# Optimization experiments

Measured on AMD Instinct MI355X. Metric: run time of the kernel, lower is better.

Reference implementation:

```python
import jax, jax.numpy as jnp
import numpy as np

B, K, W = 16, 64, 2048
D, DH, DFF, NL, V = 512, 256, 2048, 4, 32001
LN_EPS = 1e-5


def _ln(x, g, b):
    mu = jnp.mean(x, axis=-1, keepdims=True)
    var = jnp.mean(jnp.square(x - mu), axis=-1, keepdims=True)
    return (x - mu) * jax.lax.rsqrt(var + LN_EPS) * g + b


def setup_inputs() -> dict:
    key = jax.random.key(0)
    ks = iter(jax.random.split(key, 64))
    nrm = lambda shape, s=0.02: (jax.random.normal(next(ks), shape, dtype=jnp.float32) * s)
    inp = {
        "cache": jax.random.randint(next(ks), (B, K), 0, V),
        "seq": jax.random.randint(next(ks), (B, W), 0, V),
        "item_embed": nrm((V, D)),
        "cache_pos_embed": nrm((K, D)),
        "seq_pos_embed": nrm((W, D)),
        "segment_embed": nrm((2, D)),
        # per-layer stacked params (leading dim NL)
        "wq_s": nrm((NL, D, DH)), "wk_s": nrm((NL, D, DH)), "wv_s": nrm((NL, D, DH)),
        "wq_c": nrm((NL, D, DH)), "wk_c": nrm((NL, D, DH)), "wv_c": nrm((NL, D, DH)),
        "w_out": nrm((NL, D, D)), "b_out": jnp.zeros((NL, D), jnp.float32),
        "ln1_g": jnp.ones((NL, D), jnp.float32), "ln1_b": jnp.zeros((NL, D), jnp.float32),
        "ln2_g": jnp.ones((NL, D), jnp.float32), "ln2_b": jnp.zeros((NL, D), jnp.float32),
        "w_ff1": nrm((NL, D, DFF)), "b_ff1": jnp.zeros((NL, DFF), jnp.float32),
        "w_ff2": nrm((NL, DFF, D)), "b_ff2": jnp.zeros((NL, D), jnp.float32),
        "fin_g": jnp.ones((D,), jnp.float32), "fin_b": jnp.zeros((D,), jnp.float32),
        "w_ev": nrm((D, 1)), "b_ev": jnp.zeros((1,), jnp.float32),
    }
    return inp


def _forward(cache, seq, item_embed, cache_pos_embed, seq_pos_embed, segment_embed,
             wq_s, wk_s, wv_s, wq_c, wk_c, wv_c, w_out, b_out,
             ln1_g, ln1_b, ln2_g, ln2_b, w_ff1, b_ff1, w_ff2, b_ff2,
             fin_g, fin_b, w_ev, b_ev):
    scale = 1.0 / jnp.sqrt(jnp.float32(DH))
    cache_emb = item_embed[cache] + cache_pos_embed[None, :, :] + segment_embed[0]
    seq_emb = item_embed[seq] + seq_pos_embed[None, :, :] + segment_embed[1]
    h = jnp.concatenate([cache_emb, seq_emb], axis=1)  # (B, K+W, D)
    L = K + W
    # additive mask for stream a: cache rows attend to all seq tokens,
    # seq rows are causal within the window.  (L, W)
    causal = jnp.triu(jnp.full((W, W), -jnp.inf, dtype=jnp.float32), k=1)
    mask_a = jnp.concatenate([jnp.zeros((K, W), jnp.float32), causal], axis=0)

    for l in range(NL):
        hn = _ln(h, ln1_g[l], ln1_b[l])
        hn_seq = hn[:, K:]
        hn_cache = hn[:, :K]
        # stream a: all tokens query the sequence window (causal for seq rows)
        q_a = hn @ wq_s[l]
        k_a = hn_seq @ wk_s[l]
        v_a = hn_seq @ wv_s[l]
        scores_a = jnp.einsum('bld,bwd->blw', q_a, k_a) * scale + mask_a
        out_a = jnp.einsum('blw,bwd->bld', jax.nn.softmax(scores_a, axis=-1), v_a)
        # stream b: all tokens query the cache slots (full attention)
        q_b = hn @ wq_c[l]
        k_b = hn_cache @ wk_c[l]
        v_b = hn_cache @ wv_c[l]
        scores_b = jnp.einsum('bld,bkd->blk', q_b, k_b) * scale
        out_b = jnp.einsum('blk,bkd->bld', jax.nn.softmax(scores_b, axis=-1), v_b)
        attn_out = jnp.concatenate([out_a, out_b], axis=-1)  # (B, L, D)
        h = h + attn_out @ w_out[l] + b_out[l]
        hn2 = _ln(h, ln2_g[l], ln2_b[l])
        h = h + jax.nn.relu(hn2 @ w_ff1[l] + b_ff1[l]) @ w_ff2[l] + b_ff2[l]

    h = _ln(h, fin_g, fin_b)
    logits = (h[:, :K] @ w_ev + b_ev)[..., 0]  # (B, K)
    return logits


def reference(cache, seq, item_embed, cache_pos_embed, seq_pos_embed, segment_embed,
              wq_s, wk_s, wv_s, wq_c, wk_c, wv_c, w_out, b_out,
              ln1_g, ln1_b, ln2_g, ln2_b, w_ff1, b_ff1, w_ff2, b_ff2,
              fin_g, fin_b, w_ev, b_ev):
    return _forward(cache, seq, item_embed, cache_pos_embed, seq_pos_embed, segment_embed,
                    wq_s, wk_s, wv_s, wq_c, wk_c, wv_c, w_out, b_out,
                    ln1_g, ln1_b, ln2_g, ln2_b, w_ff1, b_ff1, w_ff2, b_ff2,
                    fin_g, fin_b, w_ev, b_ev)
```

## Files before the change

### kernel.cpp

```cpp
#include <hip/hip_runtime.h>
#include <hip/hip_bf16.h>
#include <cstdint>

#define CB 16
#define CK 64
#define CW 2048
#define CL 2112
#define CD 512
#define CDH 256
#define CDFF 2048
#define CNL 4
#define CROWS (CB*CL)
#define NCH 2
#define RCH2 (CROWS/NCH)

typedef __attribute__((ext_vector_type(8))) short bf16x8;
typedef __attribute__((ext_vector_type(4))) float f32x4;

__device__ __forceinline__ float bf2f(unsigned short u) {
    union { unsigned int i; float f; } x; x.i = ((unsigned int)u) << 16; return x.f;
}

__device__ __forceinline__ void load_lds16(const void* g, void* l) {
    __builtin_amdgcn_global_load_lds(
        (const __attribute__((address_space(1))) void*)g,
        (__attribute__((address_space(3))) void*)l, 16, 0, 0);
}

__device__ __forceinline__ void xcd_swizzle(int& bx, int& by) {
    const int gx = gridDim.x, nwg = gx * gridDim.y;
    if ((nwg & 7) == 0) {
        const int flat = by * gx + bx;
        const int cpx = nwg >> 3;
        const int swz = (flat & 7) * cpx + (flat >> 3);
        bx = swz % gx; by = swz / gx;
    }
}

#define BM 128
#define BN 128
#define BKG 64

__global__ __launch_bounds__(256) void gemm_bt(
    const short* __restrict__ A, const short* __restrict__ Bt, void* __restrict__ C,
    const float* __restrict__ bias, int M, int N, int Kd,
    int lda, int ldb, int ldc, long sA, long sB, long sC, float scale, int epi,
    int ksplit)
{
    __shared__ short lA[2][BM * BKG];
    __shared__ short lB[2][BN * BKG];
    const int tid = threadIdx.x;
    const int wave = tid >> 6, lane = tid & 63;
    const int wy = wave >> 1, wx = wave & 1;
    const int lr = lane & 15, quad = lane >> 4;
    int bx = blockIdx.x, by = blockIdx.y;
    xcd_swizzle(bx, by);
    const int m0 = by * BM, n0 = bx * BN;
    const int z = blockIdx.z;
    const short* Ab = A + (size_t)z * sA;
    const short* Bb = Bt + (size_t)z * sB;

    f32x4 acc[4][4];
#pragma unroll
    for (int i = 0; i < 4; i++)
#pragma unroll
        for (int j = 0; j < 4; j++) acc[i][j] = (f32x4){0.f, 0.f, 0.f, 0.f};

    const int sRow = lane >> 3;
    const int sCol = (((lane & 7) ^ sRow) << 3);

    int kbeg = 0, kend = Kd;
    if (ksplit > 1) { const int kc = Kd / ksplit; kbeg = z * kc; kend = kbeg + kc; }
    const int nsteps = (kend - kbeg) / BKG;

    auto stage = [&](int buf, int k0) {
#pragma unroll
        for (int n = 0; n < 4; ++n) {
            const int c = wave * 4 + n;
            int ar = m0 + c * 8 + sRow; if (ar > M - 1) ar = M - 1;
            load_lds16(Ab + (size_t)ar * lda + k0 + sCol, &lA[buf][c * 512]);
            int br = n0 + c * 8 + sRow; if (br > N - 1) br = N - 1;
            load_lds16(Bb + (size_t)br * ldb + k0 + sCol, &lB[buf][c * 512]);
        }
    };

    stage(0, kbeg);
    for (int t = 0; t < nsteps; ++t) {
        const int cur = t & 1;
        if (t + 1 < nsteps) {
            stage(cur ^ 1, kbeg + (t + 1) * BKG);
            asm volatile("s_waitcnt vmcnt(8)\n\ts_barrier" ::: "memory");
        } else {
            asm volatile("s_waitcnt vmcnt(0)\n\ts_barrier" ::: "memory");
        }
#pragma unroll
        for (int kk = 0; kk < BKG; kk += 32) {
            const int k4 = kk >> 3;
            bf16x8 av[4], bv[4];
#pragma unroll
            for (int i = 0; i < 4; i++) {
                const int ri = wy * 64 + i * 16 + lr;
                av[i] = *(const bf16x8*)&lA[cur][ri * BKG + ((((k4 + quad) ^ (ri & 7)) << 3))];
            }
#pragma unroll
            for (int j = 0; j < 4; j++) {
                const int rj = wx * 64 + j * 16 + lr;
                bv[j] = *(const bf16x8*)&lB[cur][rj * BKG + ((((k4 + quad) ^ (rj & 7)) << 3))];
            }
#pragma unroll
            for (int i = 0; i < 4; i++)
#pragma unroll
                for (int j = 0; j < 4; j++)
                    acc[i][j] = __builtin_amdgcn_mfma_f32_16x16x32_bf16(av[i], bv[j], acc[i][j], 0, 0, 0);
        }
        asm volatile("s_barrier" ::: "memory");
    }

    const int colBase = n0 + wx * 64 + lr;
    if (epi == 3) {
        float* Cp = (float*)C + (size_t)z * sC;
#pragma unroll
        for (int i = 0; i < 4; i++) {
            const int row0 = m0 + wy * 64 + i * 16 + quad * 4;
#pragma unroll
            for (int j = 0; j < 4; j++) {
                const int col = colBase + j * 16;
                if (col >= N) continue;
                const float bv_ = bias ? bias[col] : 0.f;
#pragma unroll
                for (int r = 0; r < 4; r++) {
                    const int row = row0 + r;
                    if (row < M) Cp[(size_t)row * ldc + col] += acc[i][j][r] + bv_;
                }
            }
        }
    } else {
        __hip_bfloat16* Cp = (__hip_bfloat16*)C + (size_t)z * sC;
#pragma unroll
        for (int i = 0; i < 4; i++) {
            const int row0 = m0 + wy * 64 + i * 16 + quad * 4;
#pragma unroll
            for (int j = 0; j < 4; j++) {
                const int col = colBase + j * 16;
                if (col >= N) continue;
                const float bv_ = (epi == 1) ? bias[col] : 0.f;
#pragma unroll
                for (int r = 0; r < 4; r++) {
                    const int row = row0 + r;
                    if (row < M) {
                        float v = acc[i][j][r];
                        if (epi == 1) { v += bv_; v = v > 0.f ? v : 0.f; }
                        else if (epi == 2) v *= scale;
                        Cp[(size_t)row * ldc + col] = __float2bfloat16(v);
                    }
                }
            }
        }
    }
}

__global__ __launch_bounds__(256, 2) void flash_a(
    const short* __restrict__ q,
    const short* __restrict__ ka,
    const short* __restrict__ vt,
    short* __restrict__ out)
{
    __shared__ short kbuf[64 * 256];
    __shared__ short vbuf[256 * 64];
    __shared__ short pbuf[64 * 64];
    const int tid = threadIdx.x, wave = tid >> 6, lane = tid & 63;
    const int lr = lane & 15, quad = lane >> 4;

    const int id = blockIdx.x;
    const int x = id & 7, k = id >> 3;
    const int b = 2 * x + (k >= 33);
    const int mi = (k >= 33) ? (k - 33) : k;
    const int mt = (mi == 0) ? 0 : (33 - mi);
    const int m0 = mt * 64;
    const short* kab = ka + (size_t)b * 2048 * 256;
    const short* vtb = vt + (size_t)b * 256 * 2048;

    const int nkt = (mt == 0) ? 32 : mt;

    bf16x8 qf[8];
    {
        const int qr = m0 + wave * 16 + lr;
        const short* p0 = q + ((size_t)b * CL + qr) * 512;
#pragma unroll
        for (int s = 0; s < 8; ++s) qf[s] = *(const bf16x8*)(p0 + s * 32 + quad * 8);
    }

    auto stageK = [&](int kt) {
#pragma unroll
        for (int u = 0; u < 8; ++u) {
            const int seg = u * 4 + wave;
            const int idx = seg * 64 + lane;
            const int row = idx >> 5, cp = idx & 31;
            const int cs = cp ^ (row & 7);
            load_lds16(kab + (size_t)(kt * 64 + row) * 256 + cs * 8, kbuf + seg * 512);
        }
    };
    auto stageV = [&](int kt) {
#pragma unroll
        for (int u = 0; u < 8; ++u) {
            const int seg = u * 4 + wave;
            const int idx = seg * 64 + lane;
            const int row = idx >> 3, cp = idx & 7;
            const int cs = cp ^ (row & 7);
            load_lds16(vtb + (size_t)row * 2048 + kt * 64 + cs * 8, vbuf + seg * 512);
        }
    };

    f32x4 acc_o[16];
#pragma unroll
    for (int jd = 0; jd < 16; jd++) acc_o[jd] = (f32x4){0.f, 0.f, 0.f, 0.f};
    float m_run[4], l_run[4];
    int limit[4];
#pragma unroll
    for (int rr = 0; rr < 4; rr++) {
        m_run[rr] = -1e30f; l_run[rr] = 0.f;
        const int trow = m0 + wave * 16 + quad * 4 + rr;
        limit[rr] = (trow < CK) ? CW : (trow - (CK - 1));
    }

    for (int kt = 0; kt < nkt; ++kt) {
        stageK(kt);
        stageV(kt);
        __syncthreads();

        f32x4 s_[4];
#pragma unroll
        for (int j = 0; j < 4; j++) s_[j] = (f32x4){0.f, 0.f, 0.f, 0.f};
#pragma unroll
        for (int s = 0; s < 8; ++s) {
#pragma unroll
            for (int j = 0; j < 4; ++j) {
                const int rj = j * 16 + lr;
                const bf16x8 bv = *(const bf16x8*)&kbuf[rj * 256 + (((s * 4 + quad) ^ (rj & 7)) << 3)];
                s_[j] = __builtin_amdgcn_mfma_f32_16x16x32_bf16(qf[s], bv, s_[j], 0, 0, 0);
            }
        }

        const int kbase = kt * 64;
        float tmax[4];
#pragma unroll
        for (int rr = 0; rr < 4; rr++) tmax[rr] = -1e30f;
#pragma unroll
        for (int j = 0; j < 4; j++) {
            const int key = kbase + j * 16 + lr;
#pragma unroll
            for (int rr = 0; rr < 4; rr++) {
                const float v = (key < limit[rr]) ? s_[j][rr] * 0.0625f : -1e30f;
                s_[j][rr] = v;
                tmax[rr] = fmaxf(tmax[rr], v);
            }
        }
#pragma unroll
        for (int rr = 0; rr < 4; rr++) {
#pragma unroll
            for (int off = 1; off < 16; off <<= 1)
                tmax[rr] = fmaxf(tmax[rr], __shfl_xor(tmax[rr], off));
        }
        float scal[4], rowsum[4];
#pragma unroll
        for (int rr = 0; rr < 4; rr++) {
            const float mn = fmaxf(m_run[rr], tmax[rr]);
            scal[rr] = __expf(m_run[rr] - mn);
            m_run[rr] = mn;
            rowsum[rr] = 0.f;
        }
#pragma unroll
        for (int j = 0; j < 4; j++) {
            const int cch = j * 2 + (lr >> 3);
#pragma unroll
            for (int rr = 0; rr < 4; rr++) {
                const float e = __expf(s_[j][rr] - m_run[rr]);
                rowsum[rr] += e;
                const float eo = __shfl_xor(e, 1);
                const __hip_bfloat16 b0 = __float2bfloat16(e);
                const __hip_bfloat16 b1 = __float2bfloat16(eo);
                const unsigned pk = ((unsigned)(*(const unsigned short*)&b1) << 16)
                                  | (unsigned)(*(const unsigned short*)&b0);
                if (!(lane & 1)) {
                    const int prow = wave * 16 + quad * 4 + rr;
                    *(unsigned*)&pbuf[prow * 64 + ((cch ^ (prow & 7)) << 3) + (lr & 6)] = pk;
                }
            }
        }
#pragma unroll
        for (int rr = 0; rr < 4; rr++) {
#pragma unroll
            for (int off = 1; off < 16; off <<= 1)
                rowsum[rr] += __shfl_xor(rowsum[rr], off);
            l_run[rr] = l_run[rr] * scal[rr] + rowsum[rr];
        }
#pragma unroll
        for (int jd = 0; jd < 16; jd++)
#pragma unroll
            for (int rr = 0; rr < 4; rr++) acc_o[jd][rr] *= scal[rr];


        const int pr = wave * 16 + lr;
#pragma unroll
        for (int s2 = 0; s2 < 2; ++s2) {
            const bf16x8 pa = *(const bf16x8*)&pbuf[pr * 64 + (((s2 * 4 + quad) ^ (pr & 7)) << 3)];
#pragma unroll
            for (int jd = 0; jd < 16; ++jd) {
                const int rj = jd * 16 + lr;
                const bf16x8 bv = *(const bf16x8*)&vbuf[rj * 64 + (((s2 * 4 + quad) ^ (rj & 7)) << 3)];
                acc_o[jd] = __builtin_amdgcn_mfma_f32_16x16x32_bf16(pa, bv, acc_o[jd], 0, 0, 0);
            }
        }
        __syncthreads();
    }

#pragma unroll
    for (int rr = 0; rr < 4; rr++) {
        const int trow = m0 + wave * 16 + quad * 4 + rr;
        const float rinv = 1.f / l_run[rr];
        __hip_bfloat16* op = (__hip_bfloat16*)out + ((size_t)b * CL + trow) * CD;
#pragma unroll
        for (int jd = 0; jd < 16; jd++)
            op[jd * 16 + lr] = __float2bfloat16(acc_o[jd][rr] * rinv);
    }
}

__global__ void embed_kernel(const int* __restrict__ cache, const int* __restrict__ seq,
                             const float* __restrict__ item, const float* __restrict__ cpos,
                             const float* __restrict__ spos, const float* __restrict__ seg,
                             float* __restrict__ h)
{
    const int row = blockIdx.x;
    const int b = row / CL, t = row - b * CL;
    const int d = threadIdx.x * 4;
    int id; const float* pos; const float* sg;
    if (t < CK) { id = cache[b * CK + t]; pos = cpos + (size_t)t * CD; sg = seg; }
    else { const int tt = t - CK; id = seq[b * CW + tt]; pos = spos + (size_t)tt * CD; sg = seg + CD; }
    const float4 ev = *(const float4*)(item + (size_t)id * CD + d);
    const float4 pv = *(const float4*)(pos + d);
    const float4 sv = *(const float4*)(sg + d);
    float4 r; r.x = ev.x + pv.x + sv.x; r.y = ev.y + pv.y + sv.y;
    r.z = ev.z + pv.z + sv.z; r.w = ev.w + pv.w + sv.w;
    *(float4*)(h + (size_t)row * CD + d) = r;
}

__global__ __launch_bounds__(256) void ln_kernel(const float* __restrict__ h, const float* __restrict__ g,
                                                 const float* __restrict__ bb, __hip_bfloat16* __restrict__ out)
{
    const int row = blockIdx.x * 4 + (threadIdx.x >> 6);
    const int lane = threadIdx.x & 63;
    const float* x = h + (size_t)row * CD + lane * 8;
    const float4 a = *(const float4*)(x);
    const float4 c = *(const float4*)(x + 4);
    float s  = a.x + a.y + a.z + a.w + c.x + c.y + c.z + c.w;
    float s2 = a.x*a.x + a.y*a.y + a.z*a.z + a.w*a.w
             + c.x*c.x + c.y*c.y + c.z*c.z + c.w*c.w;
#pragma unroll
    for (int off = 32; off; off >>= 1) {
        s  += __shfl_xor(s, off);
        s2 += __shfl_xor(s2, off);
    }
    const float mu = s * (1.f / CD);
    const float var = s2 * (1.f / CD) - mu * mu;
    const float rs = rsqrtf(var + 1e-5f);
    const float4 g0 = *(const float4*)(g + lane * 8);
    const float4 g1 = *(const float4*)(g + lane * 8 + 4);
    const float4 b0 = *(const float4*)(bb + lane * 8);
    const float4 b1 = *(const float4*)(bb + lane * 8 + 4);
    float v[8] = { (a.x-mu)*rs*g0.x + b0.x, (a.y-mu)*rs*g0.y + b0.y,
                   (a.z-mu)*rs*g0.z + b0.z, (a.w-mu)*rs*g0.w + b0.w,
                   (c.x-mu)*rs*g1.x + b1.x, (c.y-mu)*rs*g1.y + b1.y,
                   (c.z-mu)*rs*g1.z + b1.z, (c.w-mu)*rs*g1.w + b1.w };
    bf16x8 ov;
#pragma unroll
    for (int kk = 0; kk < 8; kk++) {
        const __hip_bfloat16 hb = __float2bfloat16(v[kk]);
        ov[kk] = *(const short*)&hb;
    }
    *(bf16x8*)(out + (size_t)row * CD + lane * 8) = ov;
}

__global__ __launch_bounds__(256) void softmax_b_kernel(__hip_bfloat16* __restrict__ sb)
{
    const int row = blockIdx.x * 4 + (threadIdx.x >> 6);
    const int lane = threadIdx.x & 63;
    __hip_bfloat16* pr = sb + (size_t)row * 64;
    float x = __bfloat162float(pr[lane]);
    float m = x;
#pragma unroll
    for (int off = 32; off; off >>= 1) m = fmaxf(m, __shfl_xor(m, off));
    const float e = __expf(x - m);
    float s = e;
#pragma unroll
    for (int off = 32; off; off >>= 1) s += __shfl_xor(s, off);
    pr[lane] = __float2bfloat16(e / s);
}

__global__ __launch_bounds__(256) void final_kernel(const float* __restrict__ h, const float* __restrict__ g,
                                                    const float* __restrict__ bb, const float* __restrict__ wev,
                                                    const float* __restrict__ bev, float* __restrict__ out)
{
    const int idx = blockIdx.x;
    const int b = idx >> 6, t = idx & 63;
    const float* x = h + ((size_t)b * CL + t) * CD;
    const int tid = threadIdx.x, wv = tid >> 6, lane = tid & 63;
    const float2 v = *(const float2*)(x + tid * 2);
    float s = v.x + v.y, s2 = v.x * v.x + v.y * v.y;
    __shared__ float red[8];
#pragma unroll
    for (int off = 32; off; off >>= 1) { s += __shfl_down(s, off); s2 += __shfl_down(s2, off); }
    if (lane == 0) { red[wv] = s; red[4 + wv] = s2; }
    __syncthreads();
    s = red[0] + red[1] + red[2] + red[3];
    s2 = red[4] + red[5] + red[6] + red[7];
    const float mu = s * (1.f / CD);
    const float var = s2 * (1.f / CD) - mu * mu;
    const float rs = rsqrtf(var + 1e-5f);
    const float2 gg = *(const float2*)(g + tid * 2);
    const float2 bv = *(const float2*)(bb + tid * 2);
    const float2 wv2 = *(const float2*)(wev + tid * 2);
    float val = ((v.x - mu) * rs * gg.x + bv.x) * wv2.x + ((v.y - mu) * rs * gg.y + bv.y) * wv2.y;
#pragma unroll
    for (int off = 32; off; off >>= 1) val += __shfl_down(val, off);
    __syncthreads();
    if (lane == 0) red[wv] = val;
    __syncthreads();
    if (tid == 0) out[idx] = red[0] + red[1] + red[2] + red[3] + bev[0];
}

__global__ void transpose_f32(const float* __restrict__ in, __hip_bfloat16* __restrict__ out,
                              int R, int Cc, long inzs, long outzs)
{
    __shared__ float tile[32][33];
    const size_t zi = (size_t)blockIdx.z * inzs;
    const size_t zo = (size_t)blockIdx.z * outzs;
    const int c0 = blockIdx.x * 32, r0 = blockIdx.y * 32;
    const int tx = threadIdx.x, ty = threadIdx.y;
#pragma unroll
    for (int i = ty; i < 32; i += 8)
        tile[i][tx] = in[zi + (size_t)(r0 + i) * Cc + c0 + tx];
    __syncthreads();
#pragma unroll
    for (int i = ty; i < 32; i += 8)
        out[zo + (size_t)(c0 + i) * R + r0 + tx] = __float2bfloat16(tile[tx][i]);
}

extern "C" void kernel_launch(void* const* d_in, const int* in_sizes, int n_in,
                              void* d_out, int out_size, void* d_ws, size_t ws_size,
                              hipStream_t stream)
{
    const int*   cache = (const int*)d_in[0];
    const int*   seq   = (const int*)d_in[1];
    const float* item  = (const float*)d_in[2];
    const float* cpos  = (const float*)d_in[3];
    const float* spos  = (const float*)d_in[4];
    const float* seg   = (const float*)d_in[5];
    const float* wq_s  = (const float*)d_in[6];
    const float* wk_s  = (const float*)d_in[7];
    const float* wv_s  = (const float*)d_in[8];
    const float* wq_c  = (const float*)d_in[9];
    const float* wk_c  = (const float*)d_in[10];
    const float* wv_c  = (const float*)d_in[11];
    const float* w_out = (const float*)d_in[12];
    const float* b_out = (const float*)d_in[13];
    const float* ln1_g = (const float*)d_in[14];
    const float* ln1_b = (const float*)d_in[15];
    const float* ln2_g = (const float*)d_in[16];
    const float* ln2_b = (const float*)d_in[17];
    const float* w_ff1 = (const float*)d_in[18];
    const float* b_ff1 = (const float*)d_in[19];
    const float* w_ff2 = (const float*)d_in[20];
    const float* b_ff2 = (const float*)d_in[21];
    const float* fin_g = (const float*)d_in[22];
    const float* fin_b = (const float*)d_in[23];
    const float* w_ev  = (const float*)d_in[24];
    const float* b_ev  = (const float*)d_in[25];

    char* p = (char*)d_ws;
    auto alloc = [&](size_t bytes) { char* r = p; p += (bytes + 255) & ~(size_t)255; return (void*)r; };
    float* h    = (float*)alloc((size_t)CROWS * CD * 4);
    short* hnat = (short*)alloc((size_t)CROWS * CD * 2);
    short* q    = (short*)alloc((size_t)CROWS * 512 * 2);
    short* ka   = (short*)alloc((size_t)CB * CW * CDH * 2);
    short* vt   = (short*)alloc((size_t)CB * CDH * CW * 2);
    short* kb   = (short*)alloc((size_t)CB * 64 * CDH * 2);
    short* vbT  = (short*)alloc((size_t)CB * CDH * 64 * 2);
    short* sb   = (short*)alloc((size_t)CB * CL * 64 * 2);
    short* big  = (short*)alloc((size_t)4 * CL * CW * 2);
    short* wqT  = (short*)alloc((size_t)CNL * 512 * CD * 2);
    short* wksT = (short*)alloc((size_t)CNL * CDH * CD * 2);
    short* wvsT = (short*)alloc((size_t)CNL * CDH * CD * 2);
    short* wkcT = (short*)alloc((size_t)CNL * CDH * CD * 2);
    short* wvcT = (short*)alloc((size_t)CNL * CDH * CD * 2);
    short* woT  = (short*)alloc((size_t)CNL * CD * CD * 2);
    short* wf1T = (short*)alloc((size_t)CNL * CDFF * CD * 2);
    short* wf2T = (short*)alloc((size_t)CNL * CD * CDFF * 2);
    short* ffbig = q;
    (void)big;

    const dim3 tb(32, 8);
    const long zqk = (long)CD * CDH;
    const long zqT = (long)512 * CD;
    transpose_f32<<<dim3(CDH/32, CD/32, CNL), tb, 0, stream>>>(wq_s, (__hip_bfloat16*)wqT, CD, CDH, zqk, zqT);
    transpose_f32<<<dim3(CDH/32, CD/32, CNL), tb, 0, stream>>>(wq_c, (__hip_bfloat16*)(wqT + (size_t)CDH * CD), CD, CDH, zqk, zqT);
    transpose_f32<<<dim3(CDH/32, CD/32, CNL), tb, 0, stream>>>(wk_s, (__hip_bfloat16*)wksT, CD, CDH, zqk, zqk);
    transpose_f32<<<dim3(CDH/32, CD/32, CNL), tb, 0, stream>>>(wv_s, (__hip_bfloat16*)wvsT, CD, CDH, zqk, zqk);
    transpose_f32<<<dim3(CDH/32, CD/32, CNL), tb, 0, stream>>>(wk_c, (__hip_bfloat16*)wkcT, CD, CDH, zqk, zqk);
    transpose_f32<<<dim3(CDH/32, CD/32, CNL), tb, 0, stream>>>(wv_c, (__hip_bfloat16*)wvcT, CD, CDH, zqk, zqk);
    transpose_f32<<<dim3(CD/32, CD/32, CNL), tb, 0, stream>>>(w_out, (__hip_bfloat16*)woT, CD, CD, (long)CD*CD, (long)CD*CD);
    transpose_f32<<<dim3(CDFF/32, CD/32, CNL), tb, 0, stream>>>(w_ff1, (__hip_bfloat16*)wf1T, CD, CDFF, (long)CD*CDFF, (long)CD*CDFF);
    transpose_f32<<<dim3(CD/32, CDFF/32, CNL), tb, 0, stream>>>(w_ff2, (__hip_bfloat16*)wf2T, CDFF, CD, (long)CD*CDFF, (long)CD*CDFF);

    embed_kernel<<<CROWS, 128, 0, stream>>>(cache, seq, item, cpos, spos, seg, h);

    const int mtilesR = CROWS / 128;
    const int mtilesL = (CL + 127) / 128;

    for (int l = 0; l < CNL; ++l) {
        const short* wqTl  = wqT  + (size_t)l * 512 * CD;
        const short* wksTl = wksT + (size_t)l * CDH * CD;
        const short* wvsTl = wvsT + (size_t)l * CDH * CD;
        const short* wkcTl = wkcT + (size_t)l * CDH * CD;
        const short* wvcTl = wvcT + (size_t)l * CDH * CD;
        const short* woTl  = woT  + (size_t)l * CD * CD;
        const short* wf1Tl = wf1T + (size_t)l * CDFF * CD;
        const short* wf2Tl = wf2T + (size_t)l * CD * CDFF;

        ln_kernel<<<CROWS / 4, 256, 0, stream>>>(h, ln1_g + l * CD, ln1_b + l * CD, (__hip_bfloat16*)hnat);

        gemm_bt<<<dim3(512/128, mtilesR, 1), 256, 0, stream>>>(hnat, wqTl, q, nullptr,
            CROWS, 512, CD, CD, CD, 512, 0, 0, 0, 1.f, 0, 1);
        gemm_bt<<<dim3(CDH/128, CW/128, CB), 256, 0, stream>>>(hnat + (size_t)CK * CD, wksTl, ka, nullptr,
            CW, CDH, CD, CD, CD, CDH, (long)CL * CD, 0, (long)CW * CDH, 1.f, 0, 1);
        gemm_bt<<<dim3(CDH/128, 1, CB), 256, 0, stream>>>(hnat, wkcTl, kb, nullptr,
            64, CDH, CD, CD, CD, CDH, (long)CL * CD, 0, (long)64 * CDH, 1.f, 0, 1);
        gemm_bt<<<dim3(1, CDH/128, CB), 256, 0, stream>>>(wvcTl, hnat, vbT, nullptr,
            CDH, 64, CD, CD, CD, 64, 0, (long)CL * CD, (long)CDH * 64, 1.f, 0, 1);
        gemm_bt<<<dim3(CW/128, CDH/128, CB), 256, 0, stream>>>(wvsTl, hnat + (size_t)CK * CD, vt, nullptr,
            CDH, CW, CD, CD, CD, CW, 0, (long)CL * CD, (long)CDH * CW, 1.f, 0, 1);

        gemm_bt<<<dim3(1, mtilesL, CB), 256, 0, stream>>>(q + CDH, kb, sb, nullptr,
            CL, 64, CDH, 512, CDH, 64, (long)CL * 512, (long)64 * CDH, (long)CL * 64, 0.0625f, 2, 1);
        softmax_b_kernel<<<(CB * CL) / 4, 256, 0, stream>>>((__hip_bfloat16*)sb);
        gemm_bt<<<dim3(CDH/128, mtilesL, CB), 256, 0, stream>>>(sb, vbT, hnat + CDH, nullptr,
            CL, CDH, 64, 64, 64, CD, (long)CL * 64, (long)CDH * 64, (long)CL * CD, 1.f, 0, 1);

        flash_a<<<dim3(528), 256, 0, stream>>>(q, ka, vt, hnat);

        gemm_bt<<<dim3(CD/128, mtilesR, 1), 256, 0, stream>>>(hnat, woTl, h, b_out + l * CD,
            CROWS, CD, CD, CD, CD, CD, 0, 0, 0, 1.f, 3, 1);

        ln_kernel<<<CROWS / 4, 256, 0, stream>>>(h, ln2_g + l * CD, ln2_b + l * CD, (__hip_bfloat16*)hnat);

        for (int c = 0; c < NCH; ++c) {
            const size_t r0 = (size_t)c * RCH2;
            gemm_bt<<<dim3(CDFF/128, RCH2/128, 1), 256, 0, stream>>>(hnat + r0 * CD, wf1Tl, ffbig, b_ff1 + l * CDFF,
                RCH2, CDFF, CD, CD, CD, CDFF, 0, 0, 0, 1.f, 1, 1);
            gemm_bt<<<dim3(CD/128, RCH2/128, 1), 256, 0, stream>>>(ffbig, wf2Tl, h + r0 * CD, b_ff2 + l * CD,
                RCH2, CD, CDFF, CDFF, CDFF, CD, 0, 0, 0, 1.f, 3, 1);
        }
    }

    final_kernel<<<CB * CK, 256, 0, stream>>>(h, fin_g, fin_b, w_ev, b_ev, (float*)d_out);
}
```

Before: 3.347 ms.

## Fuse cache-slot attention stream into the flash attention kernel

The second attention stream (queries attending to the 64 cache slots), previously computed as three launches (scores GEMM, softmax kernel, PV GEMM), now runs at the end of the flash_a kernel. Each block stages the per-batch cache K and transposed V into the already allocated LDS buffers, does a single-tile softmax in registers, and writes the second half of the attention output directly. This removes two launches per layer and the round trip of the score matrix through global memory. The cost is extra serial work in the tail of each flash block, on top of its existing load imbalance.

Result: no change. 3.305 ms, median of 2 (-1.3%).

```diff
diff --git a/kernel.cpp b/kernel.cpp
--- a/kernel.cpp
+++ b/kernel.cpp
@@ -163,6 +163,8 @@
     const short* __restrict__ q,
     const short* __restrict__ ka,
     const short* __restrict__ vt,
+    const short* __restrict__ kb,
+    const short* __restrict__ vbT,
     short* __restrict__ out)
 {
     __shared__ short kbuf[64 * 256];
@@ -179,12 +181,14 @@
     const int m0 = mt * 64;
     const short* kab = ka + (size_t)b * 2048 * 256;
     const short* vtb = vt + (size_t)b * 256 * 2048;
+    const short* kbb = kb + (size_t)b * 64 * 256;
+    const short* vbb = vbT + (size_t)b * 256 * 64;
 
     const int nkt = (mt == 0) ? 32 : mt;
 
     bf16x8 qf[8];
+    const int qr = m0 + wave * 16 + lr;
     {
-        const int qr = m0 + wave * 16 + lr;
         const short* p0 = q + ((size_t)b * CL + qr) * 512;
 #pragma unroll
         for (int s = 0; s < 8; ++s) qf[s] = *(const bf16x8*)(p0 + s * 32 + quad * 8);
@@ -208,6 +212,26 @@
             const int row = idx >> 3, cp = idx & 7;
             const int cs = cp ^ (row & 7);
             load_lds16(vtb + (size_t)row * 2048 + kt * 64 + cs * 8, vbuf + seg * 512);
+        }
+    };
+    auto stageKB = [&]() {
+#pragma unroll
+        for (int u = 0; u < 8; ++u) {
+            const int seg = u * 4 + wave;
+            const int idx = seg * 64 + lane;
+            const int row = idx >> 5, cp = idx & 31;
+            const int cs = cp ^ (row & 7);
+            load_lds16(kbb + (size_t)row * 256 + cs * 8, kbuf + seg * 512);
+        }
+    };
+    auto stageVB = [&]() {
+#pragma unroll
+        for (int u = 0; u < 8; ++u) {
+            const int seg = u * 4 + wave;
+            const int idx = seg * 64 + lane;
+            const int row = idx >> 3, cp = idx & 7;
+            const int cs = cp ^ (row & 7);
+            load_lds16(vbb + (size_t)row * 64 + cs * 8, vbuf + seg * 512);
         }
     };
 
@@ -314,6 +338,9 @@
         __syncthreads();
     }
 
+    stageKB();
+    stageVB();
+
 #pragma unroll
     for (int rr = 0; rr < 4; rr++) {
         const int trow = m0 + wave * 16 + quad * 4 + rr;
@@ -322,6 +349,92 @@
 #pragma unroll
         for (int jd = 0; jd < 16; jd++)
             op[jd * 16 + lr] = __float2bfloat16(acc_o[jd][rr] * rinv);
+    }
+
+    {
+        const short* p0 = q + ((size_t)b * CL + qr) * 512 + CDH;
+#pragma unroll
+        for (int s = 0; s < 8; ++s) qf[s] = *(const bf16x8*)(p0 + s * 32 + quad * 8);
+    }
+    __syncthreads();
+
+    {
+        f32x4 s_[4];
+#pragma unroll
+        for (int j = 0; j < 4; j++) s_[j] = (f32x4){0.f, 0.f, 0.f, 0.f};
+#pragma unroll
+        for (int s = 0; s < 8; ++s) {
+#pragma unroll
+            for (int j = 0; j < 4; ++j) {
+                const int rj = j * 16 + lr;
+                const bf16x8 bv = *(const bf16x8*)&kbuf[rj * 256 + (((s * 4 + quad) ^ (rj & 7)) << 3)];
+                s_[j] = __builtin_amdgcn_mfma_f32_16x16x32_bf16(qf[s], bv, s_[j], 0, 0, 0);
+            }
+        }
+        float tmax[4] = {-1e30f, -1e30f, -1e30f, -1e30f};
+#pragma unroll
+        for (int j = 0; j < 4; j++)
+#pragma unroll
+            for (int rr = 0; rr < 4; rr++) {
+                const float v = s_[j][rr] * 0.0625f;
+                s_[j][rr] = v;
+                tmax[rr] = fmaxf(tmax[rr], v);
+            }
+#pragma unroll
+        for (int rr = 0; rr < 4; rr++) {
+#pragma unroll
+            for (int off = 1; off < 16; off <<= 1)
+                tmax[rr] = fmaxf(tmax[rr], __shfl_xor(tmax[rr], off));
+        }
+        float rowsum[4] = {0.f, 0.f, 0.f, 0.f};
+#pragma unroll
+        for (int j = 0; j < 4; j++) {
+            const int cch = j * 2 + (lr >> 3);
+#pragma unroll
+            for (int rr = 0; rr < 4; rr++) {
+                const float e = __expf(s_[j][rr] - tmax[rr]);
+                rowsum[rr] += e;
+                const float eo = __shfl_xor(e, 1);
+                const __hip_bfloat16 b0 = __float2bfloat16(e);
+                const __hip_bfloat16 b1 = __float2bfloat16(eo);
+                const unsigned pk = ((unsigned)(*(const unsigned short*)&b1) << 16)
+                                  | (unsigned)(*(const unsigned short*)&b0);
+                if (!(lane & 1)) {
+                    const int prow = wave * 16 + quad * 4 + rr;
+                    *(unsigned*)&pbuf[prow * 64 + ((cch ^ (prow & 7)) << 3) + (lr & 6)] = pk;
+                }
+            }
+        }
+#pragma unroll
+        for (int rr = 0; rr < 4; rr++) {
+#pragma unroll
+            for (int off = 1; off < 16; off <<= 1)
+                rowsum[rr] += __shfl_xor(rowsum[rr], off);
+        }
+#pragma unroll
+        for (int jd = 0; jd < 16; jd++) acc_o[jd] = (f32x4){0.f, 0.f, 0.f, 0.f};
+
+        const int pr = wave * 16 + lr;
+#pragma unroll
+        for (int s2 = 0; s2 < 2; ++s2) {
+            const bf16x8 pa = *(const bf16x8*)&pbuf[pr * 64 + (((s2 * 4 + quad) ^ (pr & 7)) << 3)];
+#pragma unroll
+            for (int jd = 0; jd < 16; ++jd) {
+                const int rj = jd * 16 + lr;
+                const bf16x8 bv = *(const bf16x8*)&vbuf[rj * 64 + (((s2 * 4 + quad) ^ (rj & 7)) << 3)];
+                acc_o[jd] = __builtin_amdgcn_mfma_f32_16x16x32_bf16(pa, bv, acc_o[jd], 0, 0, 0);
+            }
+        }
+
+#pragma unroll
+        for (int rr = 0; rr < 4; rr++) {
+            const int trow = m0 + wave * 16 + quad * 4 + rr;
+            const float rinv = 1.f / rowsum[rr];
+            __hip_bfloat16* op = (__hip_bfloat16*)out + ((size_t)b * CL + trow) * CD + CDH;
+#pragma unroll
+            for (int jd = 0; jd < 16; jd++)
+                op[jd * 16 + lr] = __float2bfloat16(acc_o[jd][rr] * rinv);
+        }
     }
 }
 
@@ -378,22 +491,6 @@
         ov[kk] = *(const short*)&hb;
     }
     *(bf16x8*)(out + (size_t)row * CD + lane * 8) = ov;
-}
-
-__global__ __launch_bounds__(256) void softmax_b_kernel(__hip_bfloat16* __restrict__ sb)
-{
-    const int row = blockIdx.x * 4 + (threadIdx.x >> 6);
-    const int lane = threadIdx.x & 63;
-    __hip_bfloat16* pr = sb + (size_t)row * 64;
-    float x = __bfloat162float(pr[lane]);
-    float m = x;
-#pragma unroll
-    for (int off = 32; off; off >>= 1) m = fmaxf(m, __shfl_xor(m, off));
-    const float e = __expf(x - m);
-    float s = e;
-#pragma unroll
-    for (int off = 32; off; off >>= 1) s += __shfl_xor(s, off);
-    pr[lane] = __float2bfloat16(e / s);
 }
 
 __global__ __launch_bounds__(256) void final_kernel(const float* __restrict__ h, const float* __restrict__ g,
@@ -496,7 +593,7 @@
     short* wf1T = (short*)alloc((size_t)CNL * CDFF * CD * 2);
     short* wf2T = (short*)alloc((size_t)CNL * CD * CDFF * 2);
     short* ffbig = q;
-    (void)big;
+    (void)big; (void)sb;
 
     const dim3 tb(32, 8);
     const long zqk = (long)CD * CDH;
@@ -514,7 +611,6 @@
     embed_kernel<<<CROWS, 128, 0, stream>>>(cache, seq, item, cpos, spos, seg, h);
 
     const int mtilesR = CROWS / 128;
-    const int mtilesL = (CL + 127) / 128;
 
     for (int l = 0; l < CNL; ++l) {
         const short* wqTl  = wqT  + (size_t)l * 512 * CD;
@@ -539,13 +635,7 @@
         gemm_bt<<<dim3(CW/128, CDH/128, CB), 256, 0, stream>>>(wvsTl, hnat + (size_t)CK * CD, vt, nullptr,
             CDH, CW, CD, CD, CD, CW, 0, (long)CL * CD, (long)CDH * CW, 1.f, 0, 1);
 
-        gemm_bt<<<dim3(1, mtilesL, CB), 256, 0, stream>>>(q + CDH, kb, sb, nullptr,
-            CL, 64, CDH, 512, CDH, 64, (long)CL * 512, (long)64 * CDH, (long)CL * 64, 0.0625f, 2, 1);
-        softmax_b_kernel<<<(CB * CL) / 4, 256, 0, stream>>>((__hip_bfloat16*)sb);
-        gemm_bt<<<dim3(CDH/128, mtilesL, CB), 256, 0, stream>>>(sb, vbT, hnat + CDH, nullptr,
-            CL, CDH, 64, 64, 64, CD, (long)CL * 64, (long)CDH * 64, (long)CL * CD, 1.f, 0, 1);
-
-        flash_a<<<dim3(528), 256, 0, stream>>>(q, ka, vt, hnat);
+        flash_a<<<dim3(528), 256, 0, stream>>>(q, ka, vt, kb, vbT, hnat);
 
         gemm_bt<<<dim3(CD/128, mtilesR, 1), 256, 0, stream>>>(hnat, woTl, h, b_out + l * CD,
             CROWS, CD, CD, CD, CD, CD, 0, 0, 0, 1.f, 3, 1);
```
